# Performance work log

Hardware: AMD Instinct MI355X
Metric: run time of the kernel (lower is better)

Reference implementation:

```python
import jax, jax.numpy as jnp
import numpy as np

EMB_DIM = 128
WEIGHT_COL = 24

def setup_inputs() -> dict:
    key = jax.random.key(0)
    ks = jax.random.split(key, 9)
    B, S = 8, 4096
    s_in = 1.0 / np.sqrt(EMB_DIM)
    s_out = 1.0 / np.sqrt(WEIGHT_COL)
    return {
        "x": jax.random.normal(ks[0], (B, S, EMB_DIM), dtype=jnp.float32),
        "wQ": jax.random.uniform(ks[1], (EMB_DIM, WEIGHT_COL), jnp.float32, -s_in, s_in),
        "bQ": jax.random.uniform(ks[2], (WEIGHT_COL,), jnp.float32, -s_in, s_in),
        "wK": jax.random.uniform(ks[3], (EMB_DIM, WEIGHT_COL), jnp.float32, -s_in, s_in),
        "bK": jax.random.uniform(ks[4], (WEIGHT_COL,), jnp.float32, -s_in, s_in),
        "wV": jax.random.uniform(ks[5], (EMB_DIM, WEIGHT_COL), jnp.float32, -s_in, s_in),
        "bV": jax.random.uniform(ks[6], (WEIGHT_COL,), jnp.float32, -s_in, s_in),
        "wO": jax.random.uniform(ks[7], (WEIGHT_COL, EMB_DIM), jnp.float32, -s_out, s_out),
        "bO": jax.random.uniform(ks[8], (EMB_DIM,), jnp.float32, -s_out, s_out),
    }

def reference(x, wQ, bQ, wK, bK, wV, bV, wO, bO):
    # projections: [B,S,E] -> [B,S,D]
    Q = x @ wQ + bQ
    K = x @ wK + bK
    V = x @ wV + bV
    # NOTE: source scales by sqrt(emb_dim), not sqrt(weight_col)
    scale = 1.0 / np.sqrt(EMB_DIM).astype(np.float32)
    scores = jnp.einsum('bqd,bkd->bqk', Q, K) * scale  # [B,S,S]
    A = jax.nn.softmax(scores, axis=-1)
    H = jnp.einsum('bqk,bkd->bqd', A, V)               # [B,S,D]
    return H @ wO + bO                                  # [B,S,E]
```

## Files before the change

kernel.cpp:

```cpp
#include <hip/hip_runtime.h>
#include <hip/hip_fp16.h>


#define B_ 8
#define S_ 4096
#define E_ 128
#define D_ 24
#define N_ (B_ * S_)
#define SCALE 0.08838834764831845f
#define LOG2E 1.4426950408889634f

#define TK 128
#define KS_STRIDE 40
#define VS_STRIDE 136
#define HS_STRIDE 40
#define XS_STRIDE 136
#define OS_STRIDE 84

typedef __attribute__((ext_vector_type(8))) short bfrag;
typedef __attribute__((ext_vector_type(4))) float ffrag;

__device__ inline unsigned short f2bf(float f) {
    unsigned int x = __builtin_bit_cast(unsigned int, f);
    return (unsigned short)((x + 0x7fffu + ((x >> 16) & 1u)) >> 16);
}
__device__ inline unsigned int pack2h(float a, float b) {
    unsigned int ua = __builtin_bit_cast(unsigned int, a) + 0x8000u;
    unsigned int ub = __builtin_bit_cast(unsigned int, b) + 0x8000u;
    return __builtin_amdgcn_perm(ub, ua, 0x07060302);
}
__device__ inline unsigned int packh16(float a, float b) {
    return __builtin_bit_cast(unsigned int, __builtin_amdgcn_cvt_pkrtz(a, b));
}

__global__ __launch_bounds__(256) void prep_kernel(
    const float* __restrict__ wQ, const float* __restrict__ bQ,
    const float* __restrict__ wK, const float* __restrict__ bK,
    const float* __restrict__ wV, const float* __restrict__ bV,
    const float* __restrict__ wO,
    unsigned short* __restrict__ Wf, unsigned short* __restrict__ wOf,
    float* __restrict__ bqkv)
{
    const int gtid   = blockIdx.x * 256 + threadIdx.x;
    const int stride = gridDim.x * 256;
    const float qs = SCALE * LOG2E;
    for (int idx = gtid; idx < 4 * 5 * 512; idx += stride) {
        const int j    = idx & 7;
        const int lane = (idx >> 3) & 63;
        const int nt   = (idx >> 9) % 5;
        const int kt   = idx / 2560;
        const int n = nt * 16 + (lane & 15);
        const int k = kt * 32 + ((lane >> 4) << 3) + j;
        float v = 0.0f;
        if (n < 24)      v = wQ[k * 24 + n] * qs;
        else if (n < 48) v = wK[k * 24 + (n - 24)];
        else if (n < 72) v = wV[k * 24 + (n - 48)];
        Wf[idx] = f2bf(v);
    }
    for (int idx = gtid; idx < 8 * 512; idx += stride) {
        const int j    = idx & 7;
        const int lane = (idx >> 3) & 63;
        const int nt   = idx >> 9;
        const int k = ((lane >> 4) << 3) + j;
        const int e = nt * 16 + (lane & 15);
        wOf[idx] = (k < 24) ? f2bf(wO[k * 128 + e]) : (unsigned short)0;
    }
    if (gtid < 80) {
        float v = 0.0f;
        if (gtid < 24)      v = bQ[gtid] * qs;
        else if (gtid < 48) v = bK[gtid - 24];
        else if (gtid < 72) v = bV[gtid - 48];
        bqkv[gtid] = v;
    }
}

__global__ __launch_bounds__(256) void proj_kernel(
    const float* __restrict__ x, const unsigned short* __restrict__ Wf,
    const float* __restrict__ bqkv,
    unsigned short* __restrict__ Qbf, unsigned short* __restrict__ Kbf,
    unsigned short* __restrict__ Vt)
{
    __shared__ float smem[64 * OS_STRIDE];
    unsigned short* xs = (unsigned short*)smem;
    float* os = smem;

    const int tid  = threadIdx.x;
    const int lane = tid & 63;
    const int w    = tid >> 6;
    const int col  = lane & 15;
    const int quad = lane >> 4;
    const int rb   = blockIdx.x * 64;

    #pragma unroll
    for (int i = 0; i < 8; ++i) {
        const int idx = i * 256 + tid;
        const int row = idx >> 5, c4 = idx & 31;
        const float4 xv = *(const float4*)(x + (size_t)(rb + row) * 128 + c4 * 4);
        uint2 h;
        h.x = pack2h(xv.x, xv.y);
        h.y = pack2h(xv.z, xv.w);
        *(uint2*)(&xs[row * XS_STRIDE + c4 * 4]) = h;
    }

    bfrag Wfr[20];
    #pragma unroll
    for (int f = 0; f < 20; ++f)
        Wfr[f] = *(const bfrag*)(Wf + (f * 64 + lane) * 8);

    __syncthreads();

    ffrag acc[5];
    #pragma unroll
    for (int nt = 0; nt < 5; ++nt) acc[nt] = (ffrag){0.f, 0.f, 0.f, 0.f};

    #pragma unroll
    for (int kt = 0; kt < 4; ++kt) {
        const bfrag Af = *(const bfrag*)(&xs[(w * 16 + col) * XS_STRIDE + kt * 32 + quad * 8]);
        #pragma unroll
        for (int nt = 0; nt < 5; ++nt)
            acc[nt] = __builtin_amdgcn_mfma_f32_16x16x32_bf16(Af, Wfr[kt * 5 + nt], acc[nt], 0, 0, 0);
    }

    __syncthreads();

    #pragma unroll
    for (int nt = 0; nt < 5; ++nt) {
        const float bb = bqkv[nt * 16 + col];
        #pragma unroll
        for (int r = 0; r < 4; ++r)
            os[(w * 16 + quad * 4 + r) * OS_STRIDE + nt * 16 + col] = acc[nt][r] + bb;
    }
    __syncthreads();

    {
        const int half  = tid & 1;
        const int row   = (tid >> 1) & 63;
        const int isK   = tid >> 7;
        const int cbase = isK * 24;
        unsigned int pk[8];
        #pragma unroll
        for (int g = 0; g < 8; ++g) {
            const int c0 = half * 16 + g * 2;
            const float f0 = (c0     < 24) ? os[row * OS_STRIDE + cbase + c0]     : 0.0f;
            const float f1 = (c0 + 1 < 24) ? os[row * OS_STRIDE + cbase + c0 + 1] : 0.0f;
            pk[g] = pack2h(f0, f1);
        }
        unsigned short* dst = (isK ? Kbf : Qbf) + (size_t)(rb + row) * 32 + half * 16;
        *(uint4*)(dst)     = make_uint4(pk[0], pk[1], pk[2], pk[3]);
        *(uint4*)(dst + 8) = make_uint4(pk[4], pk[5], pk[6], pk[7]);
    }

    if (tid < 192) {
        const int d  = tid % 24;
        const int ch = tid / 24;
        unsigned int p[4];
        #pragma unroll
        for (int g = 0; g < 4; ++g) {
            const float f0 = os[(ch * 8 + g * 2 + 0) * OS_STRIDE + 48 + d];
            const float f1 = os[(ch * 8 + g * 2 + 1) * OS_STRIDE + 48 + d];
            p[g] = pack2h(f0, f1);
        }
        const int b = rb >> 12, s0 = rb & 4095;
        uint4* dst = (uint4*)(Vt + (((size_t)(b * 24 + d)) << 12) + s0 + ch * 8);
        *dst = make_uint4(p[0], p[1], p[2], p[3]);
    }
}

__global__ __launch_bounds__(512, 8) void attn_kernel(
    const unsigned short* __restrict__ Qbf, const unsigned short* __restrict__ Kbf,
    const unsigned short* __restrict__ Vt,
    __half* __restrict__ Opart, float* __restrict__ lpart)
{
    __shared__ unsigned short Ks[TK * KS_STRIDE];
    __shared__ unsigned short Vs[32 * VS_STRIDE];

    const int tid    = threadIdx.x;
    const int lane   = tid & 63;
    const int w      = tid >> 6;
    const int col    = lane & 15;
    const int quad   = lane >> 4;
    const int blk    = blockIdx.x;
    const int split  = blockIdx.y;
    const int nsp    = gridDim.y;
    const int kchunk = S_ / nsp;
    const int b      = blk >> 5;
    const int qbase  = blk * 128 + w * 16;

    if (tid < 16)
        *(uint4*)(&Vs[24 * VS_STRIDE + tid * 8]) =
            make_uint4(0x3F803F80u, 0x3F803F80u, 0x3F803F80u, 0x3F803F80u);

    const bfrag Qf = *(const bfrag*)(Qbf + (size_t)(qbase + col) * 32 + quad * 8);

    ffrag Ot0 = {0.f, 0.f, 0.f, 0.f};
    ffrag Ot1 = {0.f, 0.f, 0.f, 0.f};

    const unsigned short* Kbase = Kbf + ((size_t)(b * 4096) + split * kchunk) * 32;
    const unsigned short* Vbase = Vt + (size_t)(b * 24) * 4096 + split * kchunk;

    __syncthreads();

    for (int kb = 0; kb < kchunk; kb += TK) {
        {
            const int key = tid >> 2, ch = tid & 3;
            const uint4 t4 = *(const uint4*)(Kbase + (size_t)(kb + key) * 32 + ch * 8);
            const int row = (key & ~31) + (((key >> 2) & 1) << 4)
                          + (((key & 31) >> 3) << 2) + (key & 3);
            *(uint4*)(&Ks[row * KS_STRIDE + ch * 8]) = t4;
        }
        if (tid < 384) {
            const int d = tid >> 4, ch = tid & 15;
            const uint4 t4 = *(const uint4*)(Vbase + (size_t)d * 4096 + kb + ch * 8);
            *(uint4*)(&Vs[d * VS_STRIDE + ch * 8]) = t4;
        }
        __syncthreads();

        #pragma unroll
        for (int c2 = 0; c2 < 4; ++c2) {
            const bfrag Kfe = *(const bfrag*)(&Ks[(c2 * 32 + col) * KS_STRIDE + quad * 8]);
            const bfrag Kfo = *(const bfrag*)(&Ks[(c2 * 32 + 16 + col) * KS_STRIDE + quad * 8]);
            ffrag Se = {0.f, 0.f, 0.f, 0.f};
            ffrag So = {0.f, 0.f, 0.f, 0.f};
            Se = __builtin_amdgcn_mfma_f32_16x16x32_bf16(Kfe, Qf, Se, 0, 0, 0);
            So = __builtin_amdgcn_mfma_f32_16x16x32_bf16(Kfo, Qf, So, 0, 0, 0);
            union { bfrag f; unsigned int u[4]; } P;
            P.u[0] = pack2h(__builtin_amdgcn_exp2f(Se[0]), __builtin_amdgcn_exp2f(Se[1]));
            P.u[1] = pack2h(__builtin_amdgcn_exp2f(Se[2]), __builtin_amdgcn_exp2f(Se[3]));
            P.u[2] = pack2h(__builtin_amdgcn_exp2f(So[0]), __builtin_amdgcn_exp2f(So[1]));
            P.u[3] = pack2h(__builtin_amdgcn_exp2f(So[2]), __builtin_amdgcn_exp2f(So[3]));
            const bfrag Va0 = *(const bfrag*)(&Vs[col * VS_STRIDE + c2 * 32 + quad * 8]);
            const bfrag Va1 = *(const bfrag*)(&Vs[(16 + col) * VS_STRIDE + c2 * 32 + quad * 8]);
            Ot0 = __builtin_amdgcn_mfma_f32_16x16x32_bf16(Va0, P.f, Ot0, 0, 0, 0);
            Ot1 = __builtin_amdgcn_mfma_f32_16x16x32_bf16(Va1, P.f, Ot1, 0, 0, 0);
        }
        __syncthreads();
    }

    const size_t base = ((size_t)split * N_ + qbase + col) * 32;
    {
        uint2 s0;
        s0.x = packh16(Ot0[0], Ot0[1]);
        s0.y = packh16(Ot0[2], Ot0[3]);
        *(uint2*)(Opart + base + quad * 4) = s0;
    }
    if (quad < 2) {
        uint2 s1;
        s1.x = packh16(Ot1[0], Ot1[1]);
        s1.y = packh16(Ot1[2], Ot1[3]);
        *(uint2*)(Opart + base + 16 + quad * 4) = s1;
    }
    if (quad == 2)
        lpart[(size_t)split * N_ + qbase + col] = Ot1[0];
}

__global__ __launch_bounds__(256) void combine_kernel(
    const __half* __restrict__ Opart, const float* __restrict__ lpart,
    const unsigned short* __restrict__ wOf, const float* __restrict__ bO,
    float* __restrict__ out, int nsp)
{
    __shared__ unsigned short Hs[64 * HS_STRIDE];

    const int tid = threadIdx.x;
    const int qb  = blockIdx.x * 64;
    {
        const int ql = tid >> 2;
        const int c8 = (tid & 3) * 8;
        const int q  = qb + ql;
        float a[8] = {0.f, 0.f, 0.f, 0.f, 0.f, 0.f, 0.f, 0.f};
        if (c8 < 24) {
            for (int s = 0; s < nsp; ++s) {
                const __half2* p2 = (const __half2*)(Opart + ((size_t)s * N_ + q) * 32 + c8);
                #pragma unroll
                for (int j = 0; j < 4; ++j) {
                    const float2 f = __half22float2(p2[j]);
                    a[2 * j]     += f.x;
                    a[2 * j + 1] += f.y;
                }
            }
        }
        float ls = 0.f;
        for (int s = 0; s < nsp; ++s) ls += lpart[(size_t)s * N_ + q];
        const float inv = 1.0f / ls;
        uint4 pk;
        pk.x = pack2h(a[0] * inv, a[1] * inv);
        pk.y = pack2h(a[2] * inv, a[3] * inv);
        pk.z = pack2h(a[4] * inv, a[5] * inv);
        pk.w = pack2h(a[6] * inv, a[7] * inv);
        *(uint4*)(&Hs[ql * HS_STRIDE + c8]) = pk;
    }
    __syncthreads();

    const int lane = tid & 63;
    const int w    = tid >> 6;
    const int col  = lane & 15;
    const int quad = lane >> 4;
    const bfrag Hf = *(const bfrag*)(&Hs[(w * 16 + col) * HS_STRIDE + quad * 8]);
    #pragma unroll
    for (int nt = 0; nt < 8; ++nt) {
        const bfrag Wo = *(const bfrag*)(wOf + (nt * 64 + lane) * 8);
        ffrag C = {0.f, 0.f, 0.f, 0.f};
        C = __builtin_amdgcn_mfma_f32_16x16x32_bf16(Hf, Wo, C, 0, 0, 0);
        const float bo = bO[nt * 16 + col];
        #pragma unroll
        for (int r = 0; r < 4; ++r)
            out[(size_t)(qb + w * 16 + quad * 4 + r) * 128 + nt * 16 + col] = C[r] + bo;
    }
}

extern "C" void kernel_launch(void* const* d_in, const int* in_sizes, int n_in,
                              void* d_out, int out_size, void* d_ws, size_t ws_size,
                              hipStream_t stream) {
    const float* x  = (const float*)d_in[0];
    const float* wQ = (const float*)d_in[1];
    const float* bQ = (const float*)d_in[2];
    const float* wK = (const float*)d_in[3];
    const float* bK = (const float*)d_in[4];
    const float* wV = (const float*)d_in[5];
    const float* bV = (const float*)d_in[6];
    const float* wO = (const float*)d_in[7];
    const float* bO = (const float*)d_in[8];
    float* out = (float*)d_out;

    unsigned short* ws16 = (unsigned short*)d_ws;
    unsigned short* Qbf = ws16;
    unsigned short* Kbf = Qbf + (size_t)N_ * 32;
    unsigned short* Vt  = Kbf + (size_t)N_ * 32;
    unsigned short* Wf  = Vt + (size_t)B_ * 24 * S_;
    unsigned short* wOf = Wf + 4 * 5 * 512;
    float* bqkv = (float*)(wOf + 8 * 512);
    __half* Opart = (__half*)(bqkv + 80);
    const size_t baseBytes = (size_t)((char*)Opart - (char*)d_ws);

    int nsp = 4;
    while (nsp > 1) {
        const size_t need = baseBytes + (size_t)nsp * N_ * 32 * 2 + (size_t)nsp * N_ * 4;
        if (need <= ws_size) break;
        nsp >>= 1;
    }
    float* lpart = (float*)(Opart + (size_t)nsp * N_ * 32);

    prep_kernel<<<8, 256, 0, stream>>>(wQ, bQ, wK, bK, wV, bV, wO, Wf, wOf, bqkv);
    proj_kernel<<<N_ / 64, 256, 0, stream>>>(x, Wf, bqkv, Qbf, Kbf, Vt);
    attn_kernel<<<dim3(N_ / 128, nsp), 512, 0, stream>>>(Qbf, Kbf, Vt, Opart, lpart);
    combine_kernel<<<N_ / 64, 256, 0, stream>>>(Opart, lpart, wOf, bO, out, nsp);
}
```

Baseline: 122.3 us.

## Fold weight prep into proj/combine, pre-permute K, and double attention key tile

Removes the separate prep kernel: each proj block now converts QKV weights and biases into shared memory itself, and each combine block builds its bf16 wO fragments locally. The K rows are written in the permuted order the attention kernel expects, so the attention loader does plain copies without index shuffling. The attention key tile grows from 128 to 256, halving loop iterations and barriers at the cost of larger shared memory for K and V. The trade is one fewer launch against redundant weight conversion repeated in every block.

```diff
diff --git a/kernel.cpp b/kernel.cpp
--- a/kernel.cpp
+++ b/kernel.cpp
@@ -10,9 +10,9 @@
 #define SCALE 0.08838834764831845f
 #define LOG2E 1.4426950408889634f
 
-#define TK 128
+#define TK 256
 #define KS_STRIDE 40
-#define VS_STRIDE 136
+#define VS_STRIDE 264
 #define HS_STRIDE 40
 #define XS_STRIDE 136
 #define OS_STRIDE 84
@@ -33,54 +33,17 @@
     return __builtin_bit_cast(unsigned int, __builtin_amdgcn_cvt_pkrtz(a, b));
 }
 
-__global__ __launch_bounds__(256) void prep_kernel(
+__global__ __launch_bounds__(256) void proj_kernel(
+    const float* __restrict__ x,
     const float* __restrict__ wQ, const float* __restrict__ bQ,
     const float* __restrict__ wK, const float* __restrict__ bK,
     const float* __restrict__ wV, const float* __restrict__ bV,
-    const float* __restrict__ wO,
-    unsigned short* __restrict__ Wf, unsigned short* __restrict__ wOf,
-    float* __restrict__ bqkv)
-{
-    const int gtid   = blockIdx.x * 256 + threadIdx.x;
-    const int stride = gridDim.x * 256;
-    const float qs = SCALE * LOG2E;
-    for (int idx = gtid; idx < 4 * 5 * 512; idx += stride) {
-        const int j    = idx & 7;
-        const int lane = (idx >> 3) & 63;
-        const int nt   = (idx >> 9) % 5;
-        const int kt   = idx / 2560;
-        const int n = nt * 16 + (lane & 15);
-        const int k = kt * 32 + ((lane >> 4) << 3) + j;
-        float v = 0.0f;
-        if (n < 24)      v = wQ[k * 24 + n] * qs;
-        else if (n < 48) v = wK[k * 24 + (n - 24)];
-        else if (n < 72) v = wV[k * 24 + (n - 48)];
-        Wf[idx] = f2bf(v);
-    }
-    for (int idx = gtid; idx < 8 * 512; idx += stride) {
-        const int j    = idx & 7;
-        const int lane = (idx >> 3) & 63;
-        const int nt   = idx >> 9;
-        const int k = ((lane >> 4) << 3) + j;
-        const int e = nt * 16 + (lane & 15);
-        wOf[idx] = (k < 24) ? f2bf(wO[k * 128 + e]) : (unsigned short)0;
-    }
-    if (gtid < 80) {
-        float v = 0.0f;
-        if (gtid < 24)      v = bQ[gtid] * qs;
-        else if (gtid < 48) v = bK[gtid - 24];
-        else if (gtid < 72) v = bV[gtid - 48];
-        bqkv[gtid] = v;
-    }
-}
-
-__global__ __launch_bounds__(256) void proj_kernel(
-    const float* __restrict__ x, const unsigned short* __restrict__ Wf,
-    const float* __restrict__ bqkv,
     unsigned short* __restrict__ Qbf, unsigned short* __restrict__ Kbf,
     unsigned short* __restrict__ Vt)
 {
     __shared__ float smem[64 * OS_STRIDE];
+    __shared__ unsigned short WfL[4 * 5 * 512];
+    __shared__ float bqkvL[80];
     unsigned short* xs = (unsigned short*)smem;
     float* os = smem;
 
@@ -90,6 +53,28 @@
     const int col  = lane & 15;
     const int quad = lane >> 4;
     const int rb   = blockIdx.x * 64;
+    const float qs = SCALE * LOG2E;
+
+    for (int idx = tid; idx < 4 * 5 * 512; idx += 256) {
+        const int j  = idx & 7;
+        const int ln = (idx >> 3) & 63;
+        const int nt = (idx >> 9) % 5;
+        const int kt = idx / 2560;
+        const int n = nt * 16 + (ln & 15);
+        const int k = kt * 32 + ((ln >> 4) << 3) + j;
+        float v = 0.0f;
+        if (n < 24)      v = wQ[k * 24 + n] * qs;
+        else if (n < 48) v = wK[k * 24 + (n - 24)];
+        else if (n < 72) v = wV[k * 24 + (n - 48)];
+        WfL[idx] = f2bf(v);
+    }
+    if (tid < 80) {
+        float v = 0.0f;
+        if (tid < 24)      v = bQ[tid] * qs;
+        else if (tid < 48) v = bK[tid - 24];
+        else if (tid < 72) v = bV[tid - 48];
+        bqkvL[tid] = v;
+    }
 
     #pragma unroll
     for (int i = 0; i < 8; ++i) {
@@ -102,12 +87,12 @@
         *(uint2*)(&xs[row * XS_STRIDE + c4 * 4]) = h;
     }
 
+    __syncthreads();
+
     bfrag Wfr[20];
     #pragma unroll
     for (int f = 0; f < 20; ++f)
-        Wfr[f] = *(const bfrag*)(Wf + (f * 64 + lane) * 8);
-
-    __syncthreads();
+        Wfr[f] = *(const bfrag*)(&WfL[(f * 64 + lane) * 8]);
 
     ffrag acc[5];
     #pragma unroll
@@ -125,7 +110,7 @@
 
     #pragma unroll
     for (int nt = 0; nt < 5; ++nt) {
-        const float bb = bqkv[nt * 16 + col];
+        const float bb = bqkvL[nt * 16 + col];
         #pragma unroll
         for (int r = 0; r < 4; ++r)
             os[(w * 16 + quad * 4 + r) * OS_STRIDE + nt * 16 + col] = acc[nt][r] + bb;
@@ -145,7 +130,11 @@
             const float f1 = (c0 + 1 < 24) ? os[row * OS_STRIDE + cbase + c0 + 1] : 0.0f;
             pk[g] = pack2h(f0, f1);
         }
-        unsigned short* dst = (isK ? Kbf : Qbf) + (size_t)(rb + row) * 32 + half * 16;
+        const int gkey = rb + row;
+        const int kl   = gkey & 31;
+        const int gperm = (gkey & ~31) | ((kl & 4) << 2) | ((kl & 24) >> 1) | (kl & 3);
+        unsigned short* dst = isK ? (Kbf + (size_t)gperm * 32 + half * 16)
+                                  : (Qbf + (size_t)gkey  * 32 + half * 16);
         *(uint4*)(dst)     = make_uint4(pk[0], pk[1], pk[2], pk[3]);
         *(uint4*)(dst + 8) = make_uint4(pk[4], pk[5], pk[6], pk[7]);
     }
@@ -186,7 +175,7 @@
     const int b      = blk >> 5;
     const int qbase  = blk * 128 + w * 16;
 
-    if (tid < 16)
+    if (tid < 32)
         *(uint4*)(&Vs[24 * VS_STRIDE + tid * 8]) =
             make_uint4(0x3F803F80u, 0x3F803F80u, 0x3F803F80u, 0x3F803F80u);
 
@@ -201,22 +190,26 @@
     __syncthreads();
 
     for (int kb = 0; kb < kchunk; kb += TK) {
-        {
-            const int key = tid >> 2, ch = tid & 3;
+        #pragma unroll
+        for (int i = 0; i < 2; ++i) {
+            const int idx = i * 512 + tid;
+            const int key = idx >> 2, ch = idx & 3;
             const uint4 t4 = *(const uint4*)(Kbase + (size_t)(kb + key) * 32 + ch * 8);
-            const int row = (key & ~31) + (((key >> 2) & 1) << 4)
-                          + (((key & 31) >> 3) << 2) + (key & 3);
-            *(uint4*)(&Ks[row * KS_STRIDE + ch * 8]) = t4;
-        }
-        if (tid < 384) {
-            const int d = tid >> 4, ch = tid & 15;
-            const uint4 t4 = *(const uint4*)(Vbase + (size_t)d * 4096 + kb + ch * 8);
-            *(uint4*)(&Vs[d * VS_STRIDE + ch * 8]) = t4;
+            *(uint4*)(&Ks[key * KS_STRIDE + ch * 8]) = t4;
+        }
+        #pragma unroll
+        for (int i = 0; i < 2; ++i) {
+            const int u = i * 512 + tid;
+            if (u < 768) {
+                const int d = u >> 5, ch = u & 31;
+                const uint4 t4 = *(const uint4*)(Vbase + (size_t)d * 4096 + kb + ch * 8);
+                *(uint4*)(&Vs[d * VS_STRIDE + ch * 8]) = t4;
+            }
         }
         __syncthreads();
 
         #pragma unroll
-        for (int c2 = 0; c2 < 4; ++c2) {
+        for (int c2 = 0; c2 < TK / 32; ++c2) {
             const bfrag Kfe = *(const bfrag*)(&Ks[(c2 * 32 + col) * KS_STRIDE + quad * 8]);
             const bfrag Kfo = *(const bfrag*)(&Ks[(c2 * 32 + 16 + col) * KS_STRIDE + quad * 8]);
             ffrag Se = {0.f, 0.f, 0.f, 0.f};
@@ -255,13 +248,24 @@
 
 __global__ __launch_bounds__(256) void combine_kernel(
     const __half* __restrict__ Opart, const float* __restrict__ lpart,
-    const unsigned short* __restrict__ wOf, const float* __restrict__ bO,
+    const float* __restrict__ wO, const float* __restrict__ bO,
     float* __restrict__ out, int nsp)
 {
     __shared__ unsigned short Hs[64 * HS_STRIDE];
+    __shared__ unsigned short wOfL[8 * 512];
 
     const int tid = threadIdx.x;
     const int qb  = blockIdx.x * 64;
+
+    for (int idx = tid; idx < 8 * 512; idx += 256) {
+        const int j  = idx & 7;
+        const int ln = (idx >> 3) & 63;
+        const int nt = idx >> 9;
+        const int k = ((ln >> 4) << 3) + j;
+        const int e = nt * 16 + (ln & 15);
+        wOfL[idx] = (k < 24) ? f2bf(wO[k * 128 + e]) : (unsigned short)0;
+    }
+
     {
         const int ql = tid >> 2;
         const int c8 = (tid & 3) * 8;
@@ -297,7 +301,7 @@
     const bfrag Hf = *(const bfrag*)(&Hs[(w * 16 + col) * HS_STRIDE + quad * 8]);
     #pragma unroll
     for (int nt = 0; nt < 8; ++nt) {
-        const bfrag Wo = *(const bfrag*)(wOf + (nt * 64 + lane) * 8);
+        const bfrag Wo = *(const bfrag*)(&wOfL[(nt * 64 + lane) * 8]);
         ffrag C = {0.f, 0.f, 0.f, 0.f};
         C = __builtin_amdgcn_mfma_f32_16x16x32_bf16(Hf, Wo, C, 0, 0, 0);
         const float bo = bO[nt * 16 + col];
@@ -325,10 +329,7 @@
     unsigned short* Qbf = ws16;
     unsigned short* Kbf = Qbf + (size_t)N_ * 32;
     unsigned short* Vt  = Kbf + (size_t)N_ * 32;
-    unsigned short* Wf  = Vt + (size_t)B_ * 24 * S_;
-    unsigned short* wOf = Wf + 4 * 5 * 512;
-    float* bqkv = (float*)(wOf + 8 * 512);
-    __half* Opart = (__half*)(bqkv + 80);
+    __half* Opart = (__half*)(Vt + (size_t)B_ * 24 * S_);
     const size_t baseBytes = (size_t)((char*)Opart - (char*)d_ws);
 
     int nsp = 4;
@@ -339,8 +340,7 @@
     }
     float* lpart = (float*)(Opart + (size_t)nsp * N_ * 32);
 
-    prep_kernel<<<8, 256, 0, stream>>>(wQ, bQ, wK, bK, wV, bV, wO, Wf, wOf, bqkv);
-    proj_kernel<<<N_ / 64, 256, 0, stream>>>(x, Wf, bqkv, Qbf, Kbf, Vt);
+    proj_kernel<<<N_ / 64, 256, 0, stream>>>(x, wQ, bQ, wK, bK, wV, bV, Qbf, Kbf, Vt);
     attn_kernel<<<dim3(N_ / 128, nsp), 512, 0, stream>>>(Qbf, Kbf, Vt, Opart, lpart);
-    combine_kernel<<<N_ / 64, 256, 0, stream>>>(Opart, lpart, wOf, bO, out, nsp);
-}
+    combine_kernel<<<N_ / 64, 256, 0, stream>>>(Opart, lpart, wO, bO, out, nsp);
+}
```

Result: slower. 131.7 us (+7.7%).
